# Kernel optimization log

Measured on AMD Instinct MI355X. Metric: run time of the kernel, lower is better.

Reference implementation:

```python
import jax, jax.numpy as jnp
import numpy as np

HEADS, D_K = 8, 64   # dim=512 -> d_k = dim//heads = 64; with dim_head=64 the rearrange collapses to [B,H,N,d_k]
EPS = 1e-5


def _per_head_layernorm(t, g, b):
    # t: [B,H,N,D]; g,b: [H,D] (independent LayerNorm per head, biased variance like torch)
    mu = t.mean(-1, keepdims=True)
    var = ((t - mu) ** 2).mean(-1, keepdims=True)
    return (t - mu) * jax.lax.rsqrt(var + EPS) * g[None, :, None, :] + b[None, :, None, :]


def setup_inputs() -> dict:
    key = jax.random.key(0)
    k0, k1, k2, k3, k4, k5 = jax.random.split(key, 6)
    B, N, DIM = 4, 2048, 512
    inner = HEADS * D_K  # = DIM here
    x = jax.random.normal(k0, (B, N, DIM), jnp.float32)
    W_qkv = jax.random.normal(k1, (DIM, 3 * inner), jnp.float32) * (DIM ** -0.5)  # xavier-ish, no bias
    g_q = 1.0 + 0.1 * jax.random.normal(k2, (HEADS, D_K), jnp.float32)
    b_q = 0.1 * jax.random.normal(k3, (HEADS, D_K), jnp.float32)
    g_k = 1.0 + 0.1 * jax.random.normal(k4, (HEADS, D_K), jnp.float32)
    b_k = 0.1 * jax.random.normal(k5, (HEADS, D_K), jnp.float32)
    return {"x": x, "W_qkv": W_qkv, "g_q": g_q, "b_q": b_q, "g_k": g_k, "b_k": b_k}


def reference(x, W_qkv, g_q, b_q, g_k, b_k):
    B, N, _ = x.shape
    qkv = x @ W_qkv                              # [B,N,3*H*D]
    q, k, v = jnp.split(qkv, 3, axis=-1)

    def split_heads(t):
        return t.reshape(B, N, HEADS, D_K).transpose(0, 2, 1, 3)  # [B,H,N,D]

    q, k, v = map(split_heads, (q, k, v))
    q = _per_head_layernorm(q, g_q, b_q)
    k = _per_head_layernorm(k, g_k, b_k)
    # un-normalized linear attention: scale by 1/sqrt(d_k) then by 1/seq_len (no softmax)
    dots = jnp.einsum('bhnd,bhmd->bhnm', q, k) * (D_K ** -0.5)
    p_attn = dots / N
    out = jnp.einsum('bhnm,bhmd->bhnd', p_attn, v)  # [B,H,N,D]
    return out.transpose(0, 2, 1, 3).reshape(B, N, HEADS * D_K)
```

## Files before the change

### kernel.cpp

```cpp
#include <hip/hip_runtime.h>
#include <hip/hip_bf16.h>
#include <stdint.h>

using bf16   = __bf16;
using bf16x4 = __attribute__((ext_vector_type(4))) __bf16;
using bf16x8 = __attribute__((ext_vector_type(8))) __bf16;
using f32x4  = __attribute__((ext_vector_type(4))) float;

static constexpr int BATCH = 4, SEQ = 2048, DIM = 512, HEADS = 8, DK = 64;
static constexpr int M    = BATCH * SEQ;
static constexpr int NQKV = 3 * DIM;

#define GLD16(src, dst)                                                        \
    __builtin_amdgcn_global_load_lds(                                          \
        (const __attribute__((address_space(1))) void*)(src),                  \
        (__attribute__((address_space(3))) void*)(dst), 16, 0, 0)

__global__ __launch_bounds__(256) void k_prep(const float* __restrict__ w,
                                              bf16* __restrict__ wt)
{
    const int bid = blockIdx.x;
    const int t   = threadIdx.x;
    const int rt = bid / 48, ct = bid - rt * 48;
    __shared__ float tile[32][33];
    const int r = t >> 5, c = t & 31;
    #pragma unroll
    for (int i = 0; i < 4; ++i)
        tile[r + i * 8][c] = w[(rt * 32 + r + i * 8) * NQKV + ct * 32 + c];
    __syncthreads();
    #pragma unroll
    for (int i = 0; i < 4; ++i)
        wt[(ct * 32 + r + i * 8) * DIM + rt * 32 + c] = (bf16)tile[c][r + i * 8];
}

__global__ __launch_bounds__(384) void k_gemm(const float* __restrict__ x,
                                              const bf16* __restrict__ Wt,
                                              const float* __restrict__ gq,
                                              const float* __restrict__ bq,
                                              const float* __restrict__ gk,
                                              const float* __restrict__ bk,
                                              bf16* __restrict__ qn,
                                              float* __restrict__ Sp)
{
    __shared__ union {
        struct { bf16 A[128 * 64]; bf16 B[192 * 64]; } g;
        struct { bf16 q[2][64][72]; bf16 kst[64 * 128]; bf16 vst[64 * 128]; } e;
    } u;

    const int t    = threadIdx.x;
    const int lane = t & 63, wave = t >> 6;
    const int wm   = wave & 1, ws = wave >> 1;
    const int orig = blockIdx.x;
    const int wg   = (orig & 7) * 64 + (orig >> 3);
    const int mt   = wg >> 3, h = wg & 7;
    const int m0   = mt * 128;

    const int l15 = lane & 15, l4 = lane >> 4;
    const int rl  = lane >> 3, cl = (lane & 7) ^ rl;

    f32x4 acc[4][4] = {};

    for (int k0 = 0; k0 < 512; k0 += 64) {
        #pragma unroll
        for (int i = 0; i < 4; ++i) {
            const int ch  = wave * 4 + i;
            const int sec = ch >> 3;
            const int r   = (ch & 7) * 8 + rl;
            GLD16(Wt + ((sec * 512 + h * 64 + r) * 512 + k0 + cl * 8),
                  u.g.B + ch * 512);
        }
        for (int i = t; i < 2048; i += 384) {
            const int row = i >> 4, ch = i & 15;
            float4 v = *(const float4*)(x + (m0 + row) * 512 + k0 + ch * 4);
            bf16x4 o = { (bf16)v.x, (bf16)v.y, (bf16)v.z, (bf16)v.w };
            *(bf16x4*)(u.g.A + row * 64 + (((ch >> 1) ^ (row & 7)) * 8) + (ch & 1) * 4) = o;
        }
        __syncthreads();
        #pragma unroll
        for (int kh = 0; kh < 2; ++kh) {
            bf16x8 af[4], bfv[4];
            const int rc = kh * 4 + l4;
            #pragma unroll
            for (int mf = 0; mf < 4; ++mf) {
                const int row = wm * 64 + mf * 16 + l15;
                af[mf] = *(const bf16x8*)(u.g.A + row * 64 + ((rc ^ (row & 7)) * 8));
            }
            #pragma unroll
            for (int nf = 0; nf < 4; ++nf) {
                const int row = ws * 64 + nf * 16 + l15;
                bfv[nf] = *(const bf16x8*)(u.g.B + row * 64 + ((rc ^ (row & 7)) * 8));
            }
            #pragma unroll
            for (int mf = 0; mf < 4; ++mf)
                #pragma unroll
                for (int nf = 0; nf < 4; ++nf)
                    acc[mf][nf] = __builtin_amdgcn_mfma_f32_16x16x32_bf16(
                        af[mf], bfv[nf], acc[mf][nf], 0, 0, 0);
        }
        __syncthreads();
    }

    const int b  = m0 >> 11;
    const int bh = b * 8 + h;
    const int nwbase = (m0 & 2047) + wm * 64;

    if (ws < 2) {
        const float* gp = (ws == 0 ? gq : gk) + h * 64;
        const float* bp = (ws == 0 ? bq : bk) + h * 64;
        float gv[4], bv[4];
        #pragma unroll
        for (int nf = 0; nf < 4; ++nf) {
            gv[nf] = gp[nf * 16 + l15];
            bv[nf] = bp[nf * 16 + l15];
        }
        #pragma unroll
        for (int mf = 0; mf < 4; ++mf) {
            float mu[4], rs[4];
            #pragma unroll
            for (int r = 0; r < 4; ++r) {
                float s = 0.f, s2 = 0.f;
                #pragma unroll
                for (int nf = 0; nf < 4; ++nf) {
                    const float xv = acc[mf][nf][r];
                    s += xv; s2 += xv * xv;
                }
                s  += __shfl_xor(s, 1);  s  += __shfl_xor(s, 2);
                s  += __shfl_xor(s, 4);  s  += __shfl_xor(s, 8);
                s2 += __shfl_xor(s2, 1); s2 += __shfl_xor(s2, 2);
                s2 += __shfl_xor(s2, 4); s2 += __shfl_xor(s2, 8);
                mu[r] = s * (1.f / 64.f);
                rs[r] = rsqrtf(s2 * (1.f / 64.f) - mu[r] * mu[r] + 1e-5f);
            }
            #pragma unroll
            for (int nf = 0; nf < 4; ++nf) {
                bf16x4 pk;
                #pragma unroll
                for (int r = 0; r < 4; ++r)
                    pk[r] = (bf16)((acc[mf][nf][r] - mu[r]) * rs[r] * gv[nf] + bv[nf]);
                if (ws == 0) {
                    *(bf16x4*)(&u.e.q[wm][nf * 16 + l15][mf * 16 + l4 * 4]) = pk;
                } else {
                    const int d = nf * 16 + l15;
                    const int c = wm * 8 + mf * 2 + (l4 >> 1);
                    *(bf16x4*)(u.e.kst + d * 128 + ((c ^ (d & 7)) * 8) + (l4 & 1) * 4) = pk;
                }
            }
        }
    } else {
        #pragma unroll
        for (int mf = 0; mf < 4; ++mf)
            #pragma unroll
            for (int nf = 0; nf < 4; ++nf) {
                bf16x4 pk;
                #pragma unroll
                for (int r = 0; r < 4; ++r) pk[r] = (bf16)acc[mf][nf][r];
                const int d = nf * 16 + l15;
                const int c = wm * 8 + mf * 2 + (l4 >> 1);
                *(bf16x4*)(u.e.vst + d * 128 + ((c ^ (d & 7)) * 8) + (l4 & 1) * 4) = pk;
            }
    }

    if (ws == 0) {
        bf16* dst = qn + ((long)bh * SEQ + nwbase) * 64;
        const int nq = lane & 15, dq2 = lane >> 4;
        #pragma unroll
        for (int j = 0; j < 4; ++j) {
            const int d0 = (j * 4 + dq2) * 4;
            bf16x4 a0 = *(const bf16x4*)(&u.e.q[wm][d0 + 0][nq * 4]);
            bf16x4 a1 = *(const bf16x4*)(&u.e.q[wm][d0 + 1][nq * 4]);
            bf16x4 a2 = *(const bf16x4*)(&u.e.q[wm][d0 + 2][nq * 4]);
            bf16x4 a3 = *(const bf16x4*)(&u.e.q[wm][d0 + 3][nq * 4]);
            #pragma unroll
            for (int c = 0; c < 4; ++c) {
                bf16x4 o = { a0[c], a1[c], a2[c], a3[c] };
                *(bf16x4*)(dst + (nq * 4 + c) * 64 + d0) = o;
            }
        }
    }

    __syncthreads();

    if (ws == 2) {
        f32x4 sac[4][4] = {};
        #pragma unroll
        for (int kk = 0; kk < 2; ++kk) {
            const int ksi = wm * 2 + kk;
            const int c   = ksi * 4 + l4;
            bf16x8 av[4], bk8[4];
            #pragma unroll
            for (int i = 0; i < 4; ++i) {
                const int dp = i * 16 + l15;
                av[i] = *(const bf16x8*)(u.e.vst + dp * 128 + ((c ^ (dp & 7)) * 8));
            }
            #pragma unroll
            for (int j = 0; j < 4; ++j) {
                const int dd = j * 16 + l15;
                bk8[j] = *(const bf16x8*)(u.e.kst + dd * 128 + ((c ^ (dd & 7)) * 8));
            }
            #pragma unroll
            for (int i = 0; i < 4; ++i)
                #pragma unroll
                for (int j = 0; j < 4; ++j)
                    sac[i][j] = __builtin_amdgcn_mfma_f32_16x16x32_bf16(
                        av[i], bk8[j], sac[i][j], 0, 0, 0);
        }
        float* red = (float*)u.e.q;
        if (wm == 0) {
            #pragma unroll
            for (int i = 0; i < 4; ++i)
                #pragma unroll
                for (int j = 0; j < 4; ++j)
                    *(f32x4*)(red + ((i * 16 + l4 * 4) * 64 + j * 16 + l15) + 0) =
                        (f32x4){0.f, 0.f, 0.f, 0.f};
        }
        if (wm == 0) {
            #pragma unroll
            for (int i = 0; i < 4; ++i)
                #pragma unroll
                for (int j = 0; j < 4; ++j)
                    #pragma unroll
                    for (int r = 0; r < 4; ++r)
                        red[(i * 16 + l4 * 4 + r) * 64 + j * 16 + l15] = sac[i][j][r];
        }
        __builtin_amdgcn_s_barrier();
        if (wm == 1) {
            float* Sb = Sp + (long)(mt * 8 + h) * 4096;
            #pragma unroll
            for (int i = 0; i < 4; ++i)
                #pragma unroll
                for (int j = 0; j < 4; ++j)
                    #pragma unroll
                    for (int r = 0; r < 4; ++r) {
                        const int dp = i * 16 + l4 * 4 + r;
                        const int dd = j * 16 + l15;
                        Sb[dp * 64 + dd] = sac[i][j][r] + red[dp * 64 + dd];
                    }
        }
    }
}

__global__ __launch_bounds__(256) void k_out(const bf16* __restrict__ qn,
                                             const float* __restrict__ Sp,
                                             float* __restrict__ out)
{
    __shared__ float sS[64 * 68];
    const int bid = blockIdx.x;
    const int bh = bid >> 3, nt8 = bid & 7;
    const int b = bh >> 3, h = bh & 7;
    const int t = threadIdx.x, lane = t & 63, wave = t >> 6;
    const int l15 = lane & 15, l4 = lane >> 4;

    f32x4 racc[4] = {};
    for (int mt16 = 0; mt16 < 16; ++mt16) {
        const float* p = Sp + (long)(((b * 16 + mt16) * 8) + h) * 4096 + t * 4;
        #pragma unroll
        for (int j = 0; j < 4; ++j)
            racc[j] += *(const f32x4*)(p + j * 1024);
    }
    #pragma unroll
    for (int j = 0; j < 4; ++j) {
        const int f  = j * 1024 + t * 4;
        const int dp = f >> 6, dd = f & 63;
        *(f32x4*)(sS + dp * 68 + dd) = racc[j];
    }
    __syncthreads();

    const float scale = 1.f / 16384.f;
    bf16x8 bfr[2][4];
    #pragma unroll
    for (int kh = 0; kh < 2; ++kh)
        #pragma unroll
        for (int cf = 0; cf < 4; ++cf) {
            const float* p = sS + (cf * 16 + l15) * 68 + kh * 32 + l4 * 8;
            float4 lo = *(const float4*)(p);
            float4 hi = *(const float4*)(p + 4);
            bf16x8 f;
            f[0] = (bf16)(lo.x * scale); f[1] = (bf16)(lo.y * scale);
            f[2] = (bf16)(lo.z * scale); f[3] = (bf16)(lo.w * scale);
            f[4] = (bf16)(hi.x * scale); f[5] = (bf16)(hi.y * scale);
            f[6] = (bf16)(hi.z * scale); f[7] = (bf16)(hi.w * scale);
            bfr[kh][cf] = f;
        }

    const bf16* qb = qn + (long)bh * SEQ * 64;
    const int nbase = nt8 * 256 + wave * 64;

    #pragma unroll
    for (int mf = 0; mf < 4; ++mf) {
        bf16x8 a0 = *(const bf16x8*)(qb + (nbase + mf * 16 + l15) * 64 +      l4 * 8);
        bf16x8 a1 = *(const bf16x8*)(qb + (nbase + mf * 16 + l15) * 64 + 32 + l4 * 8);
        f32x4 acc[4] = {};
        #pragma unroll
        for (int cf = 0; cf < 4; ++cf) {
            acc[cf] = __builtin_amdgcn_mfma_f32_16x16x32_bf16(a0, bfr[0][cf], acc[cf], 0, 0, 0);
            acc[cf] = __builtin_amdgcn_mfma_f32_16x16x32_bf16(a1, bfr[1][cf], acc[cf], 0, 0, 0);
        }
        #pragma unroll
        for (int cf = 0; cf < 4; ++cf)
            #pragma unroll
            for (int r = 0; r < 4; ++r) {
                const int n = nbase + mf * 16 + l4 * 4 + r;
                out[((long)b * SEQ + n) * 512 + h * 64 + cf * 16 + l15] = acc[cf][r];
            }
    }
}

extern "C" void kernel_launch(void* const* d_in, const int* in_sizes, int n_in,
                              void* d_out, int out_size, void* d_ws, size_t ws_size,
                              hipStream_t stream)
{
    const float* x  = (const float*)d_in[0];
    const float* w  = (const float*)d_in[1];
    const float* gq = (const float*)d_in[2];
    const float* bq = (const float*)d_in[3];
    const float* gk = (const float*)d_in[4];
    const float* bk = (const float*)d_in[5];
    float* out = (float*)d_out;

    char* ws = (char*)d_ws;
    bf16*  wt = (bf16*)(ws);
    bf16*  qn = (bf16*)(ws + 1572864);
    float* Sp = (float*)(ws + 9961472);

    hipLaunchKernelGGL(k_prep, dim3(768), dim3(256), 0, stream, w, wt);
    hipLaunchKernelGGL(k_gemm, dim3(512), dim3(384), 0, stream,
                       x, wt, gq, bq, gk, bk, qn, Sp);
    hipLaunchKernelGGL(k_out,  dim3(256), dim3(256), 0, stream, qn, Sp, out);
}
```

Measured before the change: 119.9 us.

## Halve GEMM row tile to 64 and add separate partial-KV reduction kernel

```diff
diff --git a/kernel.cpp b/kernel.cpp
--- a/kernel.cpp
+++ b/kernel.cpp
@@ -33,7 +33,7 @@
         wt[(ct * 32 + r + i * 8) * DIM + rt * 32 + c] = (bf16)tile[c][r + i * 8];
 }
 
-__global__ __launch_bounds__(384) void k_gemm(const float* __restrict__ x,
+__global__ __launch_bounds__(192) void k_gemm(const float* __restrict__ x,
                                               const bf16* __restrict__ Wt,
                                               const float* __restrict__ gq,
                                               const float* __restrict__ bq,
@@ -43,17 +43,17 @@
                                               float* __restrict__ Sp)
 {
     __shared__ union {
-        struct { bf16 A[128 * 64]; bf16 B[192 * 64]; } g;
-        struct { bf16 q[2][64][72]; bf16 kst[64 * 128]; bf16 vst[64 * 128]; } e;
+        struct { bf16 A[64 * 64]; bf16 B[192 * 64]; } g;
+        struct { bf16 q[64][72]; bf16 kst[64 * 64]; bf16 vst[64 * 64]; } e;
     } u;
 
     const int t    = threadIdx.x;
     const int lane = t & 63, wave = t >> 6;
-    const int wm   = wave & 1, ws = wave >> 1;
+    const int ws   = wave;
     const int orig = blockIdx.x;
-    const int wg   = (orig & 7) * 64 + (orig >> 3);
+    const int wg   = (orig & 7) * 128 + (orig >> 3);
     const int mt   = wg >> 3, h = wg & 7;
-    const int m0   = mt * 128;
+    const int m0   = mt * 64;
 
     const int l15 = lane & 15, l4 = lane >> 4;
     const int rl  = lane >> 3, cl = (lane & 7) ^ rl;
@@ -62,18 +62,22 @@
 
     for (int k0 = 0; k0 < 512; k0 += 64) {
         #pragma unroll
-        for (int i = 0; i < 4; ++i) {
-            const int ch  = wave * 4 + i;
+        for (int i = 0; i < 8; ++i) {
+            const int ch  = wave * 8 + i;
             const int sec = ch >> 3;
             const int r   = (ch & 7) * 8 + rl;
             GLD16(Wt + ((sec * 512 + h * 64 + r) * 512 + k0 + cl * 8),
                   u.g.B + ch * 512);
         }
-        for (int i = t; i < 2048; i += 384) {
-            const int row = i >> 4, ch = i & 15;
-            float4 v = *(const float4*)(x + (m0 + row) * 512 + k0 + ch * 4);
-            bf16x4 o = { (bf16)v.x, (bf16)v.y, (bf16)v.z, (bf16)v.w };
-            *(bf16x4*)(u.g.A + row * 64 + (((ch >> 1) ^ (row & 7)) * 8) + (ch & 1) * 4) = o;
+        #pragma unroll
+        for (int j = 0; j < 6; ++j) {
+            const int i = t + j * 192;
+            if (i < 1024) {
+                const int row = i >> 4, ch = i & 15;
+                float4 v = *(const float4*)(x + (m0 + row) * 512 + k0 + ch * 4);
+                bf16x4 o = { (bf16)v.x, (bf16)v.y, (bf16)v.z, (bf16)v.w };
+                *(bf16x4*)(u.g.A + row * 64 + (((ch >> 1) ^ (row & 7)) * 8) + (ch & 1) * 4) = o;
+            }
         }
         __syncthreads();
         #pragma unroll
@@ -82,7 +86,7 @@
             const int rc = kh * 4 + l4;
             #pragma unroll
             for (int mf = 0; mf < 4; ++mf) {
-                const int row = wm * 64 + mf * 16 + l15;
+                const int row = mf * 16 + l15;
                 af[mf] = *(const bf16x8*)(u.g.A + row * 64 + ((rc ^ (row & 7)) * 8));
             }
             #pragma unroll
@@ -102,7 +106,7 @@
 
     const int b  = m0 >> 11;
     const int bh = b * 8 + h;
-    const int nwbase = (m0 & 2047) + wm * 64;
+    const int nwbase = m0 & 2047;
 
     if (ws < 2) {
         const float* gp = (ws == 0 ? gq : gk) + h * 64;
@@ -138,11 +142,11 @@
                 for (int r = 0; r < 4; ++r)
                     pk[r] = (bf16)((acc[mf][nf][r] - mu[r]) * rs[r] * gv[nf] + bv[nf]);
                 if (ws == 0) {
-                    *(bf16x4*)(&u.e.q[wm][nf * 16 + l15][mf * 16 + l4 * 4]) = pk;
+                    *(bf16x4*)(&u.e.q[nf * 16 + l15][mf * 16 + l4 * 4]) = pk;
                 } else {
                     const int d = nf * 16 + l15;
-                    const int c = wm * 8 + mf * 2 + (l4 >> 1);
-                    *(bf16x4*)(u.e.kst + d * 128 + ((c ^ (d & 7)) * 8) + (l4 & 1) * 4) = pk;
+                    const int c = mf * 2 + (l4 >> 1);
+                    *(bf16x4*)(u.e.kst + d * 64 + ((c ^ (d & 7)) * 8) + (l4 & 1) * 4) = pk;
                 }
             }
         }
@@ -155,8 +159,8 @@
                 #pragma unroll
                 for (int r = 0; r < 4; ++r) pk[r] = (bf16)acc[mf][nf][r];
                 const int d = nf * 16 + l15;
-                const int c = wm * 8 + mf * 2 + (l4 >> 1);
-                *(bf16x4*)(u.e.vst + d * 128 + ((c ^ (d & 7)) * 8) + (l4 & 1) * 4) = pk;
+                const int c = mf * 2 + (l4 >> 1);
+                *(bf16x4*)(u.e.vst + d * 64 + ((c ^ (d & 7)) * 8) + (l4 & 1) * 4) = pk;
             }
     }
 
@@ -166,10 +170,10 @@
         #pragma unroll
         for (int j = 0; j < 4; ++j) {
             const int d0 = (j * 4 + dq2) * 4;
-            bf16x4 a0 = *(const bf16x4*)(&u.e.q[wm][d0 + 0][nq * 4]);
-            bf16x4 a1 = *(const bf16x4*)(&u.e.q[wm][d0 + 1][nq * 4]);
-            bf16x4 a2 = *(const bf16x4*)(&u.e.q[wm][d0 + 2][nq * 4]);
-            bf16x4 a3 = *(const bf16x4*)(&u.e.q[wm][d0 + 3][nq * 4]);
+            bf16x4 a0 = *(const bf16x4*)(&u.e.q[d0 + 0][nq * 4]);
+            bf16x4 a1 = *(const bf16x4*)(&u.e.q[d0 + 1][nq * 4]);
+            bf16x4 a2 = *(const bf16x4*)(&u.e.q[d0 + 2][nq * 4]);
+            bf16x4 a3 = *(const bf16x4*)(&u.e.q[d0 + 3][nq * 4]);
             #pragma unroll
             for (int c = 0; c < 4; ++c) {
                 bf16x4 o = { a0[c], a1[c], a2[c], a3[c] };
@@ -184,18 +188,17 @@
         f32x4 sac[4][4] = {};
         #pragma unroll
         for (int kk = 0; kk < 2; ++kk) {
-            const int ksi = wm * 2 + kk;
-            const int c   = ksi * 4 + l4;
+            const int c = kk * 4 + l4;
             bf16x8 av[4], bk8[4];
             #pragma unroll
             for (int i = 0; i < 4; ++i) {
                 const int dp = i * 16 + l15;
-                av[i] = *(const bf16x8*)(u.e.vst + dp * 128 + ((c ^ (dp & 7)) * 8));
+                av[i] = *(const bf16x8*)(u.e.vst + dp * 64 + ((c ^ (dp & 7)) * 8));
             }
             #pragma unroll
             for (int j = 0; j < 4; ++j) {
                 const int dd = j * 16 + l15;
-                bk8[j] = *(const bf16x8*)(u.e.kst + dd * 128 + ((c ^ (dd & 7)) * 8));
+                bk8[j] = *(const bf16x8*)(u.e.kst + dd * 64 + ((c ^ (dd & 7)) * 8));
             }
             #pragma unroll
             for (int i = 0; i < 4; ++i)
@@ -204,43 +207,36 @@
                     sac[i][j] = __builtin_amdgcn_mfma_f32_16x16x32_bf16(
                         av[i], bk8[j], sac[i][j], 0, 0, 0);
         }
-        float* red = (float*)u.e.q;
-        if (wm == 0) {
-            #pragma unroll
-            for (int i = 0; i < 4; ++i)
-                #pragma unroll
-                for (int j = 0; j < 4; ++j)
-                    *(f32x4*)(red + ((i * 16 + l4 * 4) * 64 + j * 16 + l15) + 0) =
-                        (f32x4){0.f, 0.f, 0.f, 0.f};
-        }
-        if (wm == 0) {
-            #pragma unroll
-            for (int i = 0; i < 4; ++i)
-                #pragma unroll
-                for (int j = 0; j < 4; ++j)
-                    #pragma unroll
-                    for (int r = 0; r < 4; ++r)
-                        red[(i * 16 + l4 * 4 + r) * 64 + j * 16 + l15] = sac[i][j][r];
-        }
-        __builtin_amdgcn_s_barrier();
-        if (wm == 1) {
-            float* Sb = Sp + (long)(mt * 8 + h) * 4096;
-            #pragma unroll
-            for (int i = 0; i < 4; ++i)
-                #pragma unroll
-                for (int j = 0; j < 4; ++j)
-                    #pragma unroll
-                    for (int r = 0; r < 4; ++r) {
-                        const int dp = i * 16 + l4 * 4 + r;
-                        const int dd = j * 16 + l15;
-                        Sb[dp * 64 + dd] = sac[i][j][r] + red[dp * 64 + dd];
-                    }
-        }
-    }
+        float* Sb = Sp + (long)(mt * 8 + h) * 4096;
+        #pragma unroll
+        for (int i = 0; i < 4; ++i)
+            #pragma unroll
+            for (int j = 0; j < 4; ++j)
+                #pragma unroll
+                for (int r = 0; r < 4; ++r) {
+                    const int dp = i * 16 + l4 * 4 + r;
+                    const int dd = j * 16 + l15;
+                    Sb[dp * 64 + dd] = sac[i][j][r];
+                }
+    }
+}
+
+__global__ __launch_bounds__(256) void k_red(const float* __restrict__ Sp,
+                                             float* __restrict__ S)
+{
+    const int bid = blockIdx.x;
+    const int bh = bid >> 4, chunk = bid & 15;
+    const int b = bh >> 3, h = bh & 7;
+    const int e = chunk * 256 + threadIdx.x;
+    float s = 0.f;
+    #pragma unroll 4
+    for (int p = 0; p < 32; ++p)
+        s += Sp[((long)((b * 32 + p) * 8 + h)) * 4096 + e];
+    S[(long)bh * 4096 + e] = s;
 }
 
 __global__ __launch_bounds__(256) void k_out(const bf16* __restrict__ qn,
-                                             const float* __restrict__ Sp,
+                                             const float* __restrict__ S,
                                              float* __restrict__ out)
 {
     __shared__ float sS[64 * 68];
@@ -250,18 +246,11 @@
     const int t = threadIdx.x, lane = t & 63, wave = t >> 6;
     const int l15 = lane & 15, l4 = lane >> 4;
 
-    f32x4 racc[4] = {};
-    for (int mt16 = 0; mt16 < 16; ++mt16) {
-        const float* p = Sp + (long)(((b * 16 + mt16) * 8) + h) * 4096 + t * 4;
-        #pragma unroll
-        for (int j = 0; j < 4; ++j)
-            racc[j] += *(const f32x4*)(p + j * 1024);
-    }
     #pragma unroll
     for (int j = 0; j < 4; ++j) {
         const int f  = j * 1024 + t * 4;
         const int dp = f >> 6, dd = f & 63;
-        *(f32x4*)(sS + dp * 68 + dd) = racc[j];
+        *(f32x4*)(sS + dp * 68 + dd) = *(const f32x4*)(S + (long)bh * 4096 + f);
     }
     __syncthreads();
 
@@ -321,9 +310,11 @@
     bf16*  wt = (bf16*)(ws);
     bf16*  qn = (bf16*)(ws + 1572864);
     float* Sp = (float*)(ws + 9961472);
-
-    hipLaunchKernelGGL(k_prep, dim3(768), dim3(256), 0, stream, w, wt);
-    hipLaunchKernelGGL(k_gemm, dim3(512), dim3(384), 0, stream,
+    float* S  = (float*)(ws + 26738688);
+
+    hipLaunchKernelGGL(k_prep, dim3(768),  dim3(256), 0, stream, w, wt);
+    hipLaunchKernelGGL(k_gemm, dim3(1024), dim3(192), 0, stream,
                        x, wt, gq, bq, gk, bk, qn, Sp);
-    hipLaunchKernelGGL(k_out,  dim3(256), dim3(256), 0, stream, qn, Sp, out);
-}
+    hipLaunchKernelGGL(k_red,  dim3(512),  dim3(256), 0, stream, Sp, S);
+    hipLaunchKernelGGL(k_out,  dim3(256),  dim3(256), 0, stream, qn, S, out);
+}
```

Result: slower. 133.7 us (+11.5%).

## Load GEMM operands directly from global to registers and split partial-sum reduction

Applied to the files above, without the earlier changes.

```diff
diff --git a/kernel.cpp b/kernel.cpp
--- a/kernel.cpp
+++ b/kernel.cpp
@@ -10,11 +10,6 @@
 static constexpr int BATCH = 4, SEQ = 2048, DIM = 512, HEADS = 8, DK = 64;
 static constexpr int M    = BATCH * SEQ;
 static constexpr int NQKV = 3 * DIM;
-
-#define GLD16(src, dst)                                                        \
-    __builtin_amdgcn_global_load_lds(                                          \
-        (const __attribute__((address_space(1))) void*)(src),                  \
-        (__attribute__((address_space(3))) void*)(dst), 16, 0, 0)
 
 __global__ __launch_bounds__(256) void k_prep(const float* __restrict__ w,
                                               bf16* __restrict__ wt)
@@ -33,19 +28,18 @@
         wt[(ct * 32 + r + i * 8) * DIM + rt * 32 + c] = (bf16)tile[c][r + i * 8];
 }
 
-__global__ __launch_bounds__(384) void k_gemm(const float* __restrict__ x,
-                                              const bf16* __restrict__ Wt,
-                                              const float* __restrict__ gq,
-                                              const float* __restrict__ bq,
-                                              const float* __restrict__ gk,
-                                              const float* __restrict__ bk,
-                                              bf16* __restrict__ qn,
-                                              float* __restrict__ Sp)
-{
-    __shared__ union {
-        struct { bf16 A[128 * 64]; bf16 B[192 * 64]; } g;
-        struct { bf16 q[2][64][72]; bf16 kst[64 * 128]; bf16 vst[64 * 128]; } e;
-    } u;
+__global__ __launch_bounds__(384, 3) void k_gemm(const float* __restrict__ x,
+                                                 const bf16* __restrict__ Wt,
+                                                 const float* __restrict__ gq,
+                                                 const float* __restrict__ bq,
+                                                 const float* __restrict__ gk,
+                                                 const float* __restrict__ bk,
+                                                 bf16* __restrict__ qn,
+                                                 float* __restrict__ Sp)
+{
+    __shared__ struct {
+        bf16 q[2][64][72]; bf16 kst[64 * 128]; bf16 vst[64 * 128];
+    } e;
 
     const int t    = threadIdx.x;
     const int lane = t & 63, wave = t >> 6;
@@ -56,48 +50,40 @@
     const int m0   = mt * 128;
 
     const int l15 = lane & 15, l4 = lane >> 4;
-    const int rl  = lane >> 3, cl = (lane & 7) ^ rl;
 
     f32x4 acc[4][4] = {};
 
+    const float* xbase = x + (long)(m0 + wm * 64 + l15) * 512;
+    const bf16*  wbase = Wt + (long)(ws * 512 + h * 64 + l15) * 512;
+
     for (int k0 = 0; k0 < 512; k0 += 64) {
-        #pragma unroll
-        for (int i = 0; i < 4; ++i) {
-            const int ch  = wave * 4 + i;
-            const int sec = ch >> 3;
-            const int r   = (ch & 7) * 8 + rl;
-            GLD16(Wt + ((sec * 512 + h * 64 + r) * 512 + k0 + cl * 8),
-                  u.g.B + ch * 512);
-        }
-        for (int i = t; i < 2048; i += 384) {
-            const int row = i >> 4, ch = i & 15;
-            float4 v = *(const float4*)(x + (m0 + row) * 512 + k0 + ch * 4);
-            bf16x4 o = { (bf16)v.x, (bf16)v.y, (bf16)v.z, (bf16)v.w };
-            *(bf16x4*)(u.g.A + row * 64 + (((ch >> 1) ^ (row & 7)) * 8) + (ch & 1) * 4) = o;
-        }
-        __syncthreads();
+        bf16x8 bfv[2][4];
+        bf16x8 af[2][4];
         #pragma unroll
         for (int kh = 0; kh < 2; ++kh) {
-            bf16x8 af[4], bfv[4];
-            const int rc = kh * 4 + l4;
+            const int col = k0 + (kh * 4 + l4) * 8;
+            #pragma unroll
+            for (int nf = 0; nf < 4; ++nf)
+                bfv[kh][nf] = *(const bf16x8*)(wbase + (long)(nf * 16) * 512 + col);
             #pragma unroll
             for (int mf = 0; mf < 4; ++mf) {
-                const int row = wm * 64 + mf * 16 + l15;
-                af[mf] = *(const bf16x8*)(u.g.A + row * 64 + ((rc ^ (row & 7)) * 8));
-            }
-            #pragma unroll
-            for (int nf = 0; nf < 4; ++nf) {
-                const int row = ws * 64 + nf * 16 + l15;
-                bfv[nf] = *(const bf16x8*)(u.g.B + row * 64 + ((rc ^ (row & 7)) * 8));
-            }
+                const float* ap = xbase + (long)(mf * 16) * 512 + col;
+                float4 lo = *(const float4*)(ap);
+                float4 hi = *(const float4*)(ap + 4);
+                bf16x8 f;
+                f[0] = (bf16)lo.x; f[1] = (bf16)lo.y; f[2] = (bf16)lo.z; f[3] = (bf16)lo.w;
+                f[4] = (bf16)hi.x; f[5] = (bf16)hi.y; f[6] = (bf16)hi.z; f[7] = (bf16)hi.w;
+                af[kh][mf] = f;
+            }
+        }
+        #pragma unroll
+        for (int kh = 0; kh < 2; ++kh)
             #pragma unroll
             for (int mf = 0; mf < 4; ++mf)
                 #pragma unroll
                 for (int nf = 0; nf < 4; ++nf)
                     acc[mf][nf] = __builtin_amdgcn_mfma_f32_16x16x32_bf16(
-                        af[mf], bfv[nf], acc[mf][nf], 0, 0, 0);
-        }
-        __syncthreads();
+                        af[kh][mf], bfv[kh][nf], acc[mf][nf], 0, 0, 0);
     }
 
     const int b  = m0 >> 11;
@@ -138,11 +124,11 @@
                 for (int r = 0; r < 4; ++r)
                     pk[r] = (bf16)((acc[mf][nf][r] - mu[r]) * rs[r] * gv[nf] + bv[nf]);
                 if (ws == 0) {
-                    *(bf16x4*)(&u.e.q[wm][nf * 16 + l15][mf * 16 + l4 * 4]) = pk;
+                    *(bf16x4*)(&e.q[wm][nf * 16 + l15][mf * 16 + l4 * 4]) = pk;
                 } else {
                     const int d = nf * 16 + l15;
                     const int c = wm * 8 + mf * 2 + (l4 >> 1);
-                    *(bf16x4*)(u.e.kst + d * 128 + ((c ^ (d & 7)) * 8) + (l4 & 1) * 4) = pk;
+                    *(bf16x4*)(e.kst + d * 128 + ((c ^ (d & 7)) * 8) + (l4 & 1) * 4) = pk;
                 }
             }
         }
@@ -156,7 +142,7 @@
                 for (int r = 0; r < 4; ++r) pk[r] = (bf16)acc[mf][nf][r];
                 const int d = nf * 16 + l15;
                 const int c = wm * 8 + mf * 2 + (l4 >> 1);
-                *(bf16x4*)(u.e.vst + d * 128 + ((c ^ (d & 7)) * 8) + (l4 & 1) * 4) = pk;
+                *(bf16x4*)(e.vst + d * 128 + ((c ^ (d & 7)) * 8) + (l4 & 1) * 4) = pk;
             }
     }
 
@@ -166,10 +152,10 @@
         #pragma unroll
         for (int j = 0; j < 4; ++j) {
             const int d0 = (j * 4 + dq2) * 4;
-            bf16x4 a0 = *(const bf16x4*)(&u.e.q[wm][d0 + 0][nq * 4]);
-            bf16x4 a1 = *(const bf16x4*)(&u.e.q[wm][d0 + 1][nq * 4]);
-            bf16x4 a2 = *(const bf16x4*)(&u.e.q[wm][d0 + 2][nq * 4]);
-            bf16x4 a3 = *(const bf16x4*)(&u.e.q[wm][d0 + 3][nq * 4]);
+            bf16x4 a0 = *(const bf16x4*)(&e.q[wm][d0 + 0][nq * 4]);
+            bf16x4 a1 = *(const bf16x4*)(&e.q[wm][d0 + 1][nq * 4]);
+            bf16x4 a2 = *(const bf16x4*)(&e.q[wm][d0 + 2][nq * 4]);
+            bf16x4 a3 = *(const bf16x4*)(&e.q[wm][d0 + 3][nq * 4]);
             #pragma unroll
             for (int c = 0; c < 4; ++c) {
                 bf16x4 o = { a0[c], a1[c], a2[c], a3[c] };
@@ -190,12 +176,12 @@
             #pragma unroll
             for (int i = 0; i < 4; ++i) {
                 const int dp = i * 16 + l15;
-                av[i] = *(const bf16x8*)(u.e.vst + dp * 128 + ((c ^ (dp & 7)) * 8));
+                av[i] = *(const bf16x8*)(e.vst + dp * 128 + ((c ^ (dp & 7)) * 8));
             }
             #pragma unroll
             for (int j = 0; j < 4; ++j) {
                 const int dd = j * 16 + l15;
-                bk8[j] = *(const bf16x8*)(u.e.kst + dd * 128 + ((c ^ (dd & 7)) * 8));
+                bk8[j] = *(const bf16x8*)(e.kst + dd * 128 + ((c ^ (dd & 7)) * 8));
             }
             #pragma unroll
             for (int i = 0; i < 4; ++i)
@@ -204,15 +190,7 @@
                     sac[i][j] = __builtin_amdgcn_mfma_f32_16x16x32_bf16(
                         av[i], bk8[j], sac[i][j], 0, 0, 0);
         }
-        float* red = (float*)u.e.q;
-        if (wm == 0) {
-            #pragma unroll
-            for (int i = 0; i < 4; ++i)
-                #pragma unroll
-                for (int j = 0; j < 4; ++j)
-                    *(f32x4*)(red + ((i * 16 + l4 * 4) * 64 + j * 16 + l15) + 0) =
-                        (f32x4){0.f, 0.f, 0.f, 0.f};
-        }
+        float* red = (float*)e.q;
         if (wm == 0) {
             #pragma unroll
             for (int i = 0; i < 4; ++i)
@@ -239,29 +217,36 @@
     }
 }
 
+__global__ __launch_bounds__(256) void k_red(const float* __restrict__ Sp,
+                                             float* __restrict__ S)
+{
+    const int bid = blockIdx.x;
+    const int bh = bid >> 4, chunk = bid & 15;
+    const int b = bh >> 3, h = bh & 7;
+    const int e = chunk * 256 + threadIdx.x;
+    float s = 0.f;
+    #pragma unroll 4
+    for (int p = 0; p < 16; ++p)
+        s += Sp[((long)((b * 16 + p) * 8 + h)) * 4096 + e];
+    S[(long)bh * 4096 + e] = s;
+}
+
 __global__ __launch_bounds__(256) void k_out(const bf16* __restrict__ qn,
-                                             const float* __restrict__ Sp,
+                                             const float* __restrict__ S,
                                              float* __restrict__ out)
 {
     __shared__ float sS[64 * 68];
     const int bid = blockIdx.x;
-    const int bh = bid >> 3, nt8 = bid & 7;
+    const int bh = bid >> 4, nt16 = bid & 15;
     const int b = bh >> 3, h = bh & 7;
     const int t = threadIdx.x, lane = t & 63, wave = t >> 6;
     const int l15 = lane & 15, l4 = lane >> 4;
 
-    f32x4 racc[4] = {};
-    for (int mt16 = 0; mt16 < 16; ++mt16) {
-        const float* p = Sp + (long)(((b * 16 + mt16) * 8) + h) * 4096 + t * 4;
-        #pragma unroll
-        for (int j = 0; j < 4; ++j)
-            racc[j] += *(const f32x4*)(p + j * 1024);
-    }
     #pragma unroll
     for (int j = 0; j < 4; ++j) {
         const int f  = j * 1024 + t * 4;
         const int dp = f >> 6, dd = f & 63;
-        *(f32x4*)(sS + dp * 68 + dd) = racc[j];
+        *(f32x4*)(sS + dp * 68 + dd) = *(const f32x4*)(S + (long)bh * 4096 + f);
     }
     __syncthreads();
 
@@ -283,10 +268,10 @@
         }
 
     const bf16* qb = qn + (long)bh * SEQ * 64;
-    const int nbase = nt8 * 256 + wave * 64;
-
-    #pragma unroll
-    for (int mf = 0; mf < 4; ++mf) {
+    const int nbase = nt16 * 128 + wave * 32;
+
+    #pragma unroll
+    for (int mf = 0; mf < 2; ++mf) {
         bf16x8 a0 = *(const bf16x8*)(qb + (nbase + mf * 16 + l15) * 64 +      l4 * 8);
         bf16x8 a1 = *(const bf16x8*)(qb + (nbase + mf * 16 + l15) * 64 + 32 + l4 * 8);
         f32x4 acc[4] = {};
@@ -321,9 +306,11 @@
     bf16*  wt = (bf16*)(ws);
     bf16*  qn = (bf16*)(ws + 1572864);
     float* Sp = (float*)(ws + 9961472);
+    float* S  = (float*)(ws + 18350080);
 
     hipLaunchKernelGGL(k_prep, dim3(768), dim3(256), 0, stream, w, wt);
     hipLaunchKernelGGL(k_gemm, dim3(512), dim3(384), 0, stream,
                        x, wt, gq, bq, gk, bk, qn, Sp);
-    hipLaunchKernelGGL(k_out,  dim3(256), dim3(256), 0, stream, qn, Sp, out);
-}
+    hipLaunchKernelGGL(k_red,  dim3(512), dim3(256), 0, stream, Sp, S);
+    hipLaunchKernelGGL(k_out,  dim3(512), dim3(256), 0, stream, qn, S, out);
+}
```

New measurement: 157.5 us. 31.3% more time.

## Double-buffer QKV GEMM with larger M tile and split S reduction kernel

Applied to the files above, without the earlier changes.

```diff
diff --git a/kernel.cpp b/kernel.cpp
--- a/kernel.cpp
+++ b/kernel.cpp
@@ -15,6 +15,9 @@
     __builtin_amdgcn_global_load_lds(                                          \
         (const __attribute__((address_space(1))) void*)(src),                  \
         (__attribute__((address_space(3))) void*)(dst), 16, 0, 0)
+
+#define WAITVM(N)  asm volatile("s_waitcnt vmcnt(" #N ")" ::: "memory")
+#define WAITLGKM0  asm volatile("s_waitcnt lgkmcnt(0)" ::: "memory")
 
 __global__ __launch_bounds__(256) void k_prep(const float* __restrict__ w,
                                               bf16* __restrict__ wt)
@@ -33,7 +36,7 @@
         wt[(ct * 32 + r + i * 8) * DIM + rt * 32 + c] = (bf16)tile[c][r + i * 8];
 }
 
-__global__ __launch_bounds__(384) void k_gemm(const float* __restrict__ x,
+__global__ __launch_bounds__(768) void k_gemm(const float* __restrict__ x,
                                               const bf16* __restrict__ Wt,
                                               const float* __restrict__ gq,
                                               const float* __restrict__ bq,
@@ -43,39 +46,57 @@
                                               float* __restrict__ Sp)
 {
     __shared__ union {
-        struct { bf16 A[128 * 64]; bf16 B[192 * 64]; } g;
-        struct { bf16 q[2][64][72]; bf16 kst[64 * 128]; bf16 vst[64 * 128]; } e;
+        struct { bf16 A[2][256 * 64]; bf16 B[2][192 * 64]; } g;
+        struct { bf16 q[4][64][72]; bf16 kst[64 * 256]; bf16 vst[64 * 256]; } e;
     } u;
 
     const int t    = threadIdx.x;
     const int lane = t & 63, wave = t >> 6;
-    const int wm   = wave & 1, ws = wave >> 1;
+    const int wm   = wave & 3, ws = wave >> 2;
     const int orig = blockIdx.x;
-    const int wg   = (orig & 7) * 64 + (orig >> 3);
+    const int wg   = (orig & 7) * 32 + (orig >> 3);
     const int mt   = wg >> 3, h = wg & 7;
-    const int m0   = mt * 128;
+    const int m0   = mt * 256;
 
     const int l15 = lane & 15, l4 = lane >> 4;
     const int rl  = lane >> 3, cl = (lane & 7) ^ rl;
 
-    f32x4 acc[4][4] = {};
-
-    for (int k0 = 0; k0 < 512; k0 += 64) {
-        #pragma unroll
-        for (int i = 0; i < 4; ++i) {
-            const int ch  = wave * 4 + i;
+    auto issueA = [&](float4* areg, int k0) {
+        #pragma unroll
+        for (int j = 0; j < 6; ++j) {
+            const int i = t + j * 768;
+            if (i < 4096) {
+                const int row = i >> 4, ch = i & 15;
+                areg[j] = *(const float4*)(x + (long)(m0 + row) * 512 + k0 + ch * 4);
+            }
+        }
+    };
+    auto writeA = [&](const float4* areg, int sl) {
+        #pragma unroll
+        for (int j = 0; j < 6; ++j) {
+            const int i = t + j * 768;
+            if (i < 4096) {
+                const int row = i >> 4, ch = i & 15;
+                float4 v = areg[j];
+                bf16x4 o = { (bf16)v.x, (bf16)v.y, (bf16)v.z, (bf16)v.w };
+                *(bf16x4*)(u.g.A[sl] + row * 64 + (((ch >> 1) ^ (row & 7)) * 8)
+                           + (ch & 1) * 4) = o;
+            }
+        }
+    };
+    auto issueB = [&](int sl, int k0) {
+        #pragma unroll
+        for (int i = 0; i < 2; ++i) {
+            const int ch  = wave * 2 + i;
             const int sec = ch >> 3;
             const int r   = (ch & 7) * 8 + rl;
             GLD16(Wt + ((sec * 512 + h * 64 + r) * 512 + k0 + cl * 8),
-                  u.g.B + ch * 512);
-        }
-        for (int i = t; i < 2048; i += 384) {
-            const int row = i >> 4, ch = i & 15;
-            float4 v = *(const float4*)(x + (m0 + row) * 512 + k0 + ch * 4);
-            bf16x4 o = { (bf16)v.x, (bf16)v.y, (bf16)v.z, (bf16)v.w };
-            *(bf16x4*)(u.g.A + row * 64 + (((ch >> 1) ^ (row & 7)) * 8) + (ch & 1) * 4) = o;
-        }
-        __syncthreads();
+                  u.g.B[sl] + ch * 512);
+        }
+    };
+
+    f32x4 acc[4][4] = {};
+    auto compute = [&](int sl) {
         #pragma unroll
         for (int kh = 0; kh < 2; ++kh) {
             bf16x8 af[4], bfv[4];
@@ -83,12 +104,12 @@
             #pragma unroll
             for (int mf = 0; mf < 4; ++mf) {
                 const int row = wm * 64 + mf * 16 + l15;
-                af[mf] = *(const bf16x8*)(u.g.A + row * 64 + ((rc ^ (row & 7)) * 8));
+                af[mf] = *(const bf16x8*)(u.g.A[sl] + row * 64 + ((rc ^ (row & 7)) * 8));
             }
             #pragma unroll
             for (int nf = 0; nf < 4; ++nf) {
                 const int row = ws * 64 + nf * 16 + l15;
-                bfv[nf] = *(const bf16x8*)(u.g.B + row * 64 + ((rc ^ (row & 7)) * 8));
+                bfv[nf] = *(const bf16x8*)(u.g.B[sl] + row * 64 + ((rc ^ (row & 7)) * 8));
             }
             #pragma unroll
             for (int mf = 0; mf < 4; ++mf)
@@ -97,7 +118,40 @@
                     acc[mf][nf] = __builtin_amdgcn_mfma_f32_16x16x32_bf16(
                         af[mf], bfv[nf], acc[mf][nf], 0, 0, 0);
         }
-        __syncthreads();
+    };
+
+    {
+        float4 areg0[6];
+        issueA(areg0, 0);
+        issueB(0, 0);
+        WAITVM(2);
+        __builtin_amdgcn_sched_barrier(0);
+        writeA(areg0, 0);
+        WAITLGKM0;
+        __builtin_amdgcn_sched_barrier(0);
+    }
+
+    #pragma unroll
+    for (int st = 0; st < 8; ++st) {
+        float4 areg[6];
+        if (st < 7) {
+            issueA(areg, (st + 1) * 64);
+            issueB((st + 1) & 1, (st + 1) * 64);
+            if (wave < 4) { WAITVM(8); } else { WAITVM(7); }
+        } else {
+            WAITVM(0);
+        }
+        __builtin_amdgcn_sched_barrier(0);
+        __builtin_amdgcn_s_barrier();
+        compute(st & 1);
+        if (st < 7) {
+            WAITVM(2);
+            __builtin_amdgcn_sched_barrier(0);
+            writeA(areg, (st + 1) & 1);
+        }
+        WAITLGKM0;
+        __builtin_amdgcn_sched_barrier(0);
+        __builtin_amdgcn_s_barrier();
     }
 
     const int b  = m0 >> 11;
@@ -142,7 +196,8 @@
                 } else {
                     const int d = nf * 16 + l15;
                     const int c = wm * 8 + mf * 2 + (l4 >> 1);
-                    *(bf16x4*)(u.e.kst + d * 128 + ((c ^ (d & 7)) * 8) + (l4 & 1) * 4) = pk;
+                    *(bf16x4*)(u.e.kst + d * 256 + ((c ^ ((d & 7) << 2)) * 8)
+                               + (l4 & 1) * 4) = pk;
                 }
             }
         }
@@ -156,7 +211,8 @@
                 for (int r = 0; r < 4; ++r) pk[r] = (bf16)acc[mf][nf][r];
                 const int d = nf * 16 + l15;
                 const int c = wm * 8 + mf * 2 + (l4 >> 1);
-                *(bf16x4*)(u.e.vst + d * 128 + ((c ^ (d & 7)) * 8) + (l4 & 1) * 4) = pk;
+                *(bf16x4*)(u.e.vst + d * 256 + ((c ^ ((d & 7) << 2)) * 8)
+                           + (l4 & 1) * 4) = pk;
             }
     }
 
@@ -184,18 +240,17 @@
         f32x4 sac[4][4] = {};
         #pragma unroll
         for (int kk = 0; kk < 2; ++kk) {
-            const int ksi = wm * 2 + kk;
-            const int c   = ksi * 4 + l4;
+            const int c = (wm * 2 + kk) * 4 + l4;
             bf16x8 av[4], bk8[4];
             #pragma unroll
             for (int i = 0; i < 4; ++i) {
                 const int dp = i * 16 + l15;
-                av[i] = *(const bf16x8*)(u.e.vst + dp * 128 + ((c ^ (dp & 7)) * 8));
+                av[i] = *(const bf16x8*)(u.e.vst + dp * 256 + ((c ^ ((dp & 7) << 2)) * 8));
             }
             #pragma unroll
             for (int j = 0; j < 4; ++j) {
                 const int dd = j * 16 + l15;
-                bk8[j] = *(const bf16x8*)(u.e.kst + dd * 128 + ((c ^ (dd & 7)) * 8));
+                bk8[j] = *(const bf16x8*)(u.e.kst + dd * 256 + ((c ^ ((dd & 7) << 2)) * 8));
             }
             #pragma unroll
             for (int i = 0; i < 4; ++i)
@@ -205,25 +260,33 @@
                         av[i], bk8[j], sac[i][j], 0, 0, 0);
         }
         float* red = (float*)u.e.q;
-        if (wm == 0) {
-            #pragma unroll
-            for (int i = 0; i < 4; ++i)
-                #pragma unroll
-                for (int j = 0; j < 4; ++j)
-                    *(f32x4*)(red + ((i * 16 + l4 * 4) * 64 + j * 16 + l15) + 0) =
-                        (f32x4){0.f, 0.f, 0.f, 0.f};
-        }
-        if (wm == 0) {
+        float* r0  = red;
+        float* r1  = red + 4096;
+        if (wm < 2) {
+            float* rd = (wm == 0) ? r0 : r1;
             #pragma unroll
             for (int i = 0; i < 4; ++i)
                 #pragma unroll
                 for (int j = 0; j < 4; ++j)
                     #pragma unroll
                     for (int r = 0; r < 4; ++r)
-                        red[(i * 16 + l4 * 4 + r) * 64 + j * 16 + l15] = sac[i][j][r];
-        }
+                        rd[(i * 16 + l4 * 4 + r) * 64 + j * 16 + l15] = sac[i][j][r];
+        }
+        WAITLGKM0;
         __builtin_amdgcn_s_barrier();
-        if (wm == 1) {
+        if (wm >= 2) {
+            float* rd = (wm == 2) ? r0 : r1;
+            #pragma unroll
+            for (int i = 0; i < 4; ++i)
+                #pragma unroll
+                for (int j = 0; j < 4; ++j)
+                    #pragma unroll
+                    for (int r = 0; r < 4; ++r)
+                        rd[(i * 16 + l4 * 4 + r) * 64 + j * 16 + l15] += sac[i][j][r];
+        }
+        WAITLGKM0;
+        __builtin_amdgcn_s_barrier();
+        if (wm == 0) {
             float* Sb = Sp + (long)(mt * 8 + h) * 4096;
             #pragma unroll
             for (int i = 0; i < 4; ++i)
@@ -231,37 +294,43 @@
                 for (int j = 0; j < 4; ++j)
                     #pragma unroll
                     for (int r = 0; r < 4; ++r) {
-                        const int dp = i * 16 + l4 * 4 + r;
-                        const int dd = j * 16 + l15;
-                        Sb[dp * 64 + dd] = sac[i][j][r] + red[dp * 64 + dd];
+                        const int idx = (i * 16 + l4 * 4 + r) * 64 + j * 16 + l15;
+                        Sb[idx] = r0[idx] + r1[idx];
                     }
         }
     }
 }
 
+__global__ __launch_bounds__(256) void k_red(const float* __restrict__ Sp,
+                                             float* __restrict__ S)
+{
+    const int bid = blockIdx.x;
+    const int bh = bid >> 4, chunk = bid & 15;
+    const int b = bh >> 3, h = bh & 7;
+    const int e = chunk * 256 + threadIdx.x;
+    float s = 0.f;
+    #pragma unroll
+    for (int p = 0; p < 8; ++p)
+        s += Sp[((long)((b * 8 + p) * 8 + h)) * 4096 + e];
+    S[(long)bh * 4096 + e] = s;
+}
+
 __global__ __launch_bounds__(256) void k_out(const bf16* __restrict__ qn,
-                                             const float* __restrict__ Sp,
+                                             const float* __restrict__ S,
                                              float* __restrict__ out)
 {
     __shared__ float sS[64 * 68];
     const int bid = blockIdx.x;
-    const int bh = bid >> 3, nt8 = bid & 7;
+    const int bh = bid >> 4, nt16 = bid & 15;
     const int b = bh >> 3, h = bh & 7;
     const int t = threadIdx.x, lane = t & 63, wave = t >> 6;
     const int l15 = lane & 15, l4 = lane >> 4;
 
-    f32x4 racc[4] = {};
-    for (int mt16 = 0; mt16 < 16; ++mt16) {
-        const float* p = Sp + (long)(((b * 16 + mt16) * 8) + h) * 4096 + t * 4;
-        #pragma unroll
-        for (int j = 0; j < 4; ++j)
-            racc[j] += *(const f32x4*)(p + j * 1024);
-    }
     #pragma unroll
     for (int j = 0; j < 4; ++j) {
         const int f  = j * 1024 + t * 4;
         const int dp = f >> 6, dd = f & 63;
-        *(f32x4*)(sS + dp * 68 + dd) = racc[j];
+        *(f32x4*)(sS + dp * 68 + dd) = *(const f32x4*)(S + (long)bh * 4096 + f);
     }
     __syncthreads();
 
@@ -283,10 +352,10 @@
         }
 
     const bf16* qb = qn + (long)bh * SEQ * 64;
-    const int nbase = nt8 * 256 + wave * 64;
-
-    #pragma unroll
-    for (int mf = 0; mf < 4; ++mf) {
+    const int nbase = nt16 * 128 + wave * 32;
+
+    #pragma unroll
+    for (int mf = 0; mf < 2; ++mf) {
         bf16x8 a0 = *(const bf16x8*)(qb + (nbase + mf * 16 + l15) * 64 +      l4 * 8);
         bf16x8 a1 = *(const bf16x8*)(qb + (nbase + mf * 16 + l15) * 64 + 32 + l4 * 8);
         f32x4 acc[4] = {};
@@ -321,9 +390,11 @@
     bf16*  wt = (bf16*)(ws);
     bf16*  qn = (bf16*)(ws + 1572864);
     float* Sp = (float*)(ws + 9961472);
+    float* S  = (float*)(ws + 14155776);
 
     hipLaunchKernelGGL(k_prep, dim3(768), dim3(256), 0, stream, w, wt);
-    hipLaunchKernelGGL(k_gemm, dim3(512), dim3(384), 0, stream,
+    hipLaunchKernelGGL(k_gemm, dim3(256), dim3(768), 0, stream,
                        x, wt, gq, bq, gk, bk, qn, Sp);
-    hipLaunchKernelGGL(k_out,  dim3(256), dim3(256), 0, stream, qn, Sp, out);
+    hipLaunchKernelGGL(k_red,  dim3(512), dim3(256), 0, stream, Sp, S);
+    hipLaunchKernelGGL(k_out,  dim3(512), dim3(256), 0, stream, qn, S, out);
 }
```

After: 110.7 us. -7.7%, faster.
